# Performance work log

Hardware: AMD Instinct MI355X
Metric: run time of the kernel (lower is better)

## Reference

```python
import jax, jax.numpy as jnp
import numpy as np
import math

B, L, C, D, H, NLAYERS, DFF = 256, 100, 55, 512, 8, 3, 64


def _pos_embedding(length, d_model):
    pos = np.arange(length, dtype=np.float32)[:, None]
    div = np.exp(np.arange(0, d_model, 2, dtype=np.float32) * (-math.log(10000.0) / d_model))
    pe = np.zeros((length, d_model), dtype=np.float32)
    pe[:, 0::2] = np.sin(pos * div)
    pe[:, 1::2] = np.cos(pos * div)
    return jnp.asarray(pe)


def setup_inputs() -> dict:
    key = jax.random.key(0)
    ks = jax.random.split(key, 12)
    r = lambda k, s, sc: jax.random.normal(k, s, dtype=jnp.float32) * sc
    sD = 1.0 / math.sqrt(D)
    return {
        'x': r(ks[0], (B, L, C), 1.0),
        'tok_w': r(ks[1], (D, C, 3), 1.0 / math.sqrt(3 * C)),  # Conv1d(c_in->d_model, k=3, circular, no bias)
        'pe': _pos_embedding(L, D),
        'Wq': r(ks[2], (NLAYERS, D, D), sD), 'bq': jnp.zeros((NLAYERS, D), jnp.float32),
        'Wk': r(ks[3], (NLAYERS, D, D), sD), 'bk': jnp.zeros((NLAYERS, D), jnp.float32),
        'Wv': r(ks[4], (NLAYERS, D, D), sD), 'bv': jnp.zeros((NLAYERS, D), jnp.float32),
        'Wsig': r(ks[5], (NLAYERS, H, D), sD), 'bsig': jnp.zeros((NLAYERS, H), jnp.float32),
        'Wo': r(ks[6], (NLAYERS, D, D), sD), 'bo': jnp.zeros((NLAYERS, D), jnp.float32),
        'W1': r(ks[7], (NLAYERS, DFF, D), sD), 'b1': jnp.zeros((NLAYERS, DFF), jnp.float32),  # conv1 (1x1)
        'W2': r(ks[8], (NLAYERS, D, DFF), 1.0 / math.sqrt(DFF)), 'b2': jnp.zeros((NLAYERS, D), jnp.float32),  # conv2 (1x1)
        'proj_w': r(ks[9], (C, D), sD), 'proj_b': jnp.zeros((C,), jnp.float32),
    }


def _forward(x, tok_w, pe, Wq, bq, Wk, bk, Wv, bv, Wsig, bsig, Wo, bo, W1, b1, W2, b2, proj_w, proj_b):
    Bx, Lx, _ = x.shape
    nlayers, nH = Wsig.shape[0], Wsig.shape[1]
    d_model = Wq.shape[1]
    dk = d_model // nH
    scale = 1.0 / math.sqrt(dk)
    # token embedding: circular-padded Conv1d(k=3, no bias), then + positional embedding
    xc = jnp.pad(jnp.swapaxes(x, 1, 2), ((0, 0), (0, 0), (1, 1)), mode='wrap')  # [B,C,L+2]
    emb = jax.lax.conv_general_dilated(xc, tok_w, (1,), 'VALID', dimension_numbers=('NCW', 'OIW', 'NCW'))
    h = jnp.swapaxes(emb, 1, 2) + pe[None]  # [B,L,D]
    dist = jnp.abs(jnp.arange(Lx)[:, None] - jnp.arange(Lx)[None, :]).astype(h.dtype)  # |i-j|
    for l in range(nlayers):
        q = h @ Wq[l].T + bq[l]                       # [B,L,D]
        k = (h @ Wk[l].T + bk[l]).reshape(Bx, Lx, nH, dk)
        v = (h @ Wv[l].T + bv[l]).reshape(Bx, Lx, nH, dk)
        # NOTE: source applies sigma projection to the *projected* queries
        sigma = q @ Wsig[l].T + bsig[l]               # [B,L,H]
        qh = q.reshape(Bx, Lx, nH, dk)
        scores = jnp.einsum('blhe,bshe->bhls', qh, k)  # [B,H,L,L]
        series = jax.nn.softmax(scale * scores, axis=-1)
        # Gaussian prior branch (mask_flag=False; computed in source forward,
        # does not feed the module's returned output)
        sg = jnp.swapaxes(sigma, 1, 2)                 # [B,H,L]
        sg = jnp.power(3.0, jax.nn.sigmoid(sg * 5.0) + 1e-5) - 1.0
        sgE = sg[..., None]                            # [B,H,L,1]
        _prior = jnp.exp(-(dist ** 2)[None, None] / (2.0 * sgE ** 2)) / (math.sqrt(2.0 * math.pi) * sgE)
        o = jnp.einsum('bhls,bshd->blhd', series, v).reshape(Bx, Lx, d_model)
        h = h + (o @ Wo[l].T + bo[l])                  # residual 1 (dropout=identity at eval)
        y = jax.nn.gelu(h @ W1[l].T + b1[l], approximate=False)  # conv1 1x1 + gelu
        h = h + (y @ W2[l].T + b2[l])                  # conv2 1x1, residual 2
    return h @ proj_w.T + proj_b                       # [B,L,c_out]


def reference(x, tok_w, pe, Wq, bq, Wk, bk, Wv, bv, Wsig, bsig, Wo, bo, W1, b1, W2, b2, proj_w, proj_b):
    return _forward(x, tok_w, pe, Wq, bq, Wk, bk, Wv, bv, Wsig, bsig, Wo, bo, W1, b1, W2, b2, proj_w, proj_b)
```

## Files before the change

### kernel.cpp

```cpp
#include <hip/hip_runtime.h>
#include <stdint.h>

typedef unsigned short u16;
typedef __attribute__((ext_vector_type(8))) short short8;
typedef __attribute__((ext_vector_type(4))) float f32x4;

#define DEVI __device__ __forceinline__

#define BB   256
#define LL   100
#define CC   55
#define DD   512
#define HH   8
#define DKK  64
#define MM   (BB * LL)
#define KEMB 192
#define NSEG 17

DEVI float bf2f(u16 s) { union { unsigned int u; float f; } x; x.u = ((unsigned int)s) << 16; return x.f; }
DEVI u16 f2bf(float f) {
  union { float f; unsigned int u; } x; x.f = f;
  unsigned int u = x.u;
  return (u16)((u + 0x7FFFu + ((u >> 16) & 1u)) >> 16);
}

DEVI void async_lds16(const u16* gp, u16* lp) {
  __builtin_amdgcn_global_load_lds((const __attribute__((address_space(1))) void*)gp,
                                   (__attribute__((address_space(3))) void*)lp, 16, 0, 0);
}

DEVI void wave_lds_fence() {
  asm volatile("s_waitcnt lgkmcnt(0)" ::: "memory");
  __builtin_amdgcn_wave_barrier();
}

DEVI int swz_row(int r) { return (r & 3) ^ ((r >> 2) & 3); }

__global__ void detect_dtype(const u16* __restrict__ x, int* __restrict__ flag) {
  __shared__ int cnt[256];
  int tid = threadIdx.x;
  u16 u = x[2 * tid];
  int e = (u >> 7) & 0xFF;
  cnt[tid] = (e >= 0x5F && e <= 0x90) ? 1 : 0;
  __syncthreads();
  for (int s = 128; s > 0; s >>= 1) { if (tid < s) cnt[tid] += cnt[tid + s]; __syncthreads(); }
  if (tid == 0) *flag = (cnt[0] >= 160) ? 0 : 1;
}

struct Segs { const void* src[NSEG]; int off[NSEG + 1]; };

__global__ void convert_all(Segs s, const int* __restrict__ flag, u16* __restrict__ dst) {
  int i = blockIdx.x * 256 + threadIdx.x;
  if (i >= s.off[NSEG]) return;
  int sidx = 0;
#pragma unroll
  for (int k = 1; k < NSEG; k++) if (i >= s.off[k]) sidx = k;
  int j = i - s.off[sidx];
  u16 v;
  if (*flag) v = f2bf(((const float*)s.src[sidx])[j]);
  else       v = ((const u16*)s.src[sidx])[j];
  dst[i] = v;
}

__global__ void repack_w(const u16* __restrict__ tokw, u16* __restrict__ Wg) {
  int idx = blockIdx.x * 256 + threadIdx.x;
  if (idx >= 512 * KEMB) return;
  int d = idx / KEMB, j = idx % KEMB, k = j >> 6, c = j & 63;
  Wg[idx] = (c < CC) ? tokw[d * (CC * 3) + c * 3 + k] : (u16)0;
}

__global__ void repack_x(const u16* __restrict__ x, u16* __restrict__ Xg) {
  int idx = blockIdx.x * 256 + threadIdx.x;
  if (idx >= MM * KEMB) return;
  int m = idx / KEMB, j = idx % KEMB, k = j >> 6, c = j & 63;
  int b = m / LL, l = m % LL;
  int l2 = l + k - 1; l2 = (l2 + LL) % LL;
  Xg[idx] = (c < CC) ? x[(size_t)(b * LL + l2) * CC + c] : (u16)0;
}

struct GemmW { const u16* W[3]; const u16* bias[3]; void* out[3]; };

template<int BM, int BN, int NTT, int TAG, bool QKV, bool DIRECT>
__global__ __launch_bounds__(256)
void gemm_bt(const u16* __restrict__ A, int K, GemmW w,
             const u16* __restrict__ pe,
             const u16* __restrict__ resid,
             int dogelu,
             int ldo, int nvalid,
             const int* __restrict__ dtf)
{
  constexpr int BK = 32;
  constexpr int MI = BM / 32;
  constexpr int CW = BN / 2, NT = CW / 16;
  constexpr int SW = CW + 4;
  constexpr int STAGE_U16 = (BM + BN) * BK * 2;
  __shared__ alignas(16) u16 smem[STAGE_U16];
  u16* As = smem;
  u16* Bs = smem + BM * BK * 2;

  const int tid = threadIdx.x;
  const int lane = tid & 63;
  const int wv = __builtin_amdgcn_readfirstlane(tid >> 6);
  const int wm = wv & 1, wn = wv >> 1;
  const int l15 = lane & 15, qd = lane >> 4;
  const int swz = swz_row(l15);

  const int id = blockIdx.x;
  const int mpx = gridDim.x / (NTT * 8);
  const int xcd = id & 7, slot = id >> 3;
  const int m_t = xcd * mpx + slot / NTT;
  const int n_t = slot % NTT;
  const int m0 = m_t * BM;
  int n0 = n_t * BN;
  int sel = 0, n0l = n0;
  if (QKV) { sel = n0 >> 9; n0l = n0 & 511; }
  const u16* W = w.W[sel];
  const u16* bias = w.bias[sel];
  void* outp = w.out[sel];

  const f32x4 zf = {0.f, 0.f, 0.f, 0.f};
  f32x4 acc[MI][NT];
#pragma unroll
  for (int i = 0; i < MI; i++)
#pragma unroll
    for (int j = 0; j < NT; j++) acc[i][j] = zf;

  for (int k0 = 0; k0 < K; k0 += 2 * BK) {
    __syncthreads();
#pragma unroll
    for (int p = 0; p < 2; p++) {
      u16* Asp = As + p * BM * BK;
      u16* Bsp = Bs + p * BN * BK;
      const int kp = k0 + p * BK;
#pragma unroll
      for (int i = 0; i < BM / 64; i++) {
        int base = i * 256 + wv * 64;
        int idx = base + lane;
        int row = idx >> 2;
        int cs = ((idx & 3) ^ swz_row(row)) * 8;
        async_lds16(A + (size_t)(m0 + row) * K + kp + cs, Asp + base * 8);
      }
#pragma unroll
      for (int i = 0; i < BN / 64; i++) {
        int base = i * 256 + wv * 64;
        int idx = base + lane;
        int row = idx >> 2;
        int cs = ((idx & 3) ^ swz_row(row)) * 8;
        int gr = n0l + row; if (gr >= nvalid) gr = nvalid - 1;
        async_lds16(W + (size_t)gr * K + kp + cs, Bsp + base * 8);
      }
    }
    __syncthreads();

#pragma unroll
    for (int p = 0; p < 2; p++) {
      const u16* Asp = As + p * BM * BK;
      const u16* Bsp = Bs + p * BN * BK;
      short8 af[MI], bfr[NT];
#pragma unroll
      for (int mi = 0; mi < MI; mi++)
        af[mi] = *(const short8*)&Asp[(wm * (BM / 2) + mi * 16 + l15) * BK + ((qd ^ swz) * 8)];
#pragma unroll
      for (int ni = 0; ni < NT; ni++)
        bfr[ni] = *(const short8*)&Bsp[(wn * CW + ni * 16 + l15) * BK + ((qd ^ swz) * 8)];
#pragma unroll
      for (int mi = 0; mi < MI; mi++)
#pragma unroll
        for (int ni = 0; ni < NT; ni++)
          acc[mi][ni] = __builtin_amdgcn_mfma_f32_16x16x32_bf16(af[mi], bfr[ni], acc[mi][ni], 0, 0, 0);
    }
  }

  if (DIRECT) {
    const int sf = (dtf != nullptr) ? *dtf : 0;
#pragma unroll
    for (int mi = 0; mi < MI; mi++)
#pragma unroll
      for (int ni = 0; ni < NT; ni++) {
        int gcol = n0l + wn * CW + ni * 16 + l15;
        float bv = (bias && gcol < nvalid) ? bf2f(bias[gcol]) : 0.f;
#pragma unroll
        for (int r = 0; r < 4; r++) {
          int grow = m0 + wm * (BM / 2) + mi * 16 + qd * 4 + r;
          if (gcol < nvalid) {
            float v = acc[mi][ni][r] + bv;
            if (sf) ((float*)outp)[(size_t)grow * ldo + gcol] = v;
            else    ((u16*)outp)[(size_t)grow * ldo + gcol] = f2bf(v);
          }
        }
      }
    return;
  }

  __syncthreads();
  u16* slab = smem + wv * 16 * SW;
#pragma unroll
  for (int mi = 0; mi < MI; mi++) {
    const int lr = wm * (BM / 2) + mi * 16 + qd * 4;
    float v[NT][4];
    if (!QKV && resid) {
#pragma unroll
      for (int ni = 0; ni < NT; ni++) {
        int col = n0l + wn * CW + ni * 16 + l15;
#pragma unroll
        for (int r = 0; r < 4; r++)
          v[ni][r] = bf2f(resid[(size_t)(m0 + lr + r) * DD + col]);
      }
    } else {
#pragma unroll
      for (int ni = 0; ni < NT; ni++)
#pragma unroll
        for (int r = 0; r < 4; r++) v[ni][r] = 0.f;
    }
#pragma unroll
    for (int ni = 0; ni < NT; ni++) {
      const int lc = wn * CW + ni * 16 + l15;
      float bv = bias ? bf2f(bias[n0l + lc]) : 0.f;
#pragma unroll
      for (int r = 0; r < 4; r++) {
        float x = v[ni][r] + acc[mi][ni][r] + bv;
        if (!QKV && pe) x += bf2f(pe[((m0 + lr + r) % LL) * DD + n0l + lc]);
        if (!QKV && dogelu) x = 0.5f * x * (1.f + erff(x * 0.70710678118654752f));
        v[ni][r] = x;
      }
    }
#pragma unroll
    for (int ni = 0; ni < NT; ni++)
#pragma unroll
      for (int r = 0; r < 4; r++)
        slab[(qd * 4 + r) * SW + ni * 16 + l15] = f2bf(v[ni][r]);
    wave_lds_fence();
    if (BN == 128) {
      int r2 = lane >> 2, c2 = (lane & 3) * 16;
      int grow = m0 + wm * (BM / 2) + mi * 16 + r2;
      u16* op = (u16*)outp + (size_t)grow * ldo + n0l + wn * CW + c2;
      *(short8*)&op[0] = *(const short8*)&slab[r2 * SW + c2];
      *(short8*)&op[8] = *(const short8*)&slab[r2 * SW + c2 + 8];
    } else {
      if (lane < 32) {
        int r2 = lane >> 1, c2 = (lane & 1) * 16;
        int grow = m0 + wm * (BM / 2) + mi * 16 + r2;
        u16* op = (u16*)outp + (size_t)grow * ldo + n0l + wn * CW + c2;
        *(short8*)&op[0] = *(const short8*)&slab[r2 * SW + c2];
        *(short8*)&op[8] = *(const short8*)&slab[r2 * SW + c2 + 8];
      }
    }
    wave_lds_fence();
  }
}

__global__ __launch_bounds__(256)
void ffn_fused(const u16* __restrict__ h, const u16* __restrict__ W1,
               const u16* __restrict__ b1, const u16* __restrict__ W2,
               const u16* __restrict__ b2, u16* __restrict__ hout)
{
  constexpr int BM = 64, BK = 32, SW = 36;
  __shared__ alignas(16) u16 smem[4096 + 10496];
  u16* y      = smem;
  u16* shared = smem + 4096;
  u16* As  = shared;
  u16* Bs  = shared + 4096;
  u16* Bs2 = shared;
  u16* slabs = shared + 8192;

  const int tid = threadIdx.x;
  const int lane = tid & 63;
  const int wv = __builtin_amdgcn_readfirstlane(tid >> 6);
  const int wm = wv & 1, wn = wv >> 1;
  const int l15 = lane & 15, qd = lane >> 4;
  const int swz = swz_row(l15);
  const int id = blockIdx.x;
  const int mpx = gridDim.x >> 3;
  const int lid = (id & 7) * mpx + (id >> 3);
  const int m0 = (lid >> 1) * BM;
  const int nh = lid & 1;

  const int srow = tid >> 2;
  const int scs = ((tid & 3) ^ swz_row(srow)) * 8;
  const f32x4 zf = {0.f, 0.f, 0.f, 0.f};

  f32x4 acc[2][2];
#pragma unroll
  for (int i = 0; i < 2; i++)
#pragma unroll
    for (int j = 0; j < 2; j++) acc[i][j] = zf;

  for (int k0 = 0; k0 < DD; k0 += 64) {
    __syncthreads();
#pragma unroll
    for (int p = 0; p < 2; p++) {
      const int kp = k0 + p * BK;
      async_lds16(h  + (size_t)(m0 + srow) * DD + kp + scs, As + p * 2048 + tid * 8);
      async_lds16(W1 + (size_t)srow * DD + kp + scs,        Bs + p * 2048 + tid * 8);
    }
    __syncthreads();
#pragma unroll
    for (int p = 0; p < 2; p++) {
      short8 af[2], bfr[2];
#pragma unroll
      for (int mi = 0; mi < 2; mi++)
        af[mi] = *(const short8*)&As[p * 2048 + (wm * 32 + mi * 16 + l15) * BK + ((qd ^ swz) * 8)];
#pragma unroll
      for (int ni = 0; ni < 2; ni++)
        bfr[ni] = *(const short8*)&Bs[p * 2048 + (wn * 32 + ni * 16 + l15) * BK + ((qd ^ swz) * 8)];
#pragma unroll
      for (int mi = 0; mi < 2; mi++)
#pragma unroll
        for (int ni = 0; ni < 2; ni++)
          acc[mi][ni] = __builtin_amdgcn_mfma_f32_16x16x32_bf16(af[mi], bfr[ni], acc[mi][ni], 0, 0, 0);
    }
  }
#pragma unroll
  for (int mi = 0; mi < 2; mi++)
#pragma unroll
    for (int ni = 0; ni < 2; ni++) {
      float bv = bf2f(b1[wn * 32 + ni * 16 + l15]);
#pragma unroll
      for (int r = 0; r < 4; r++) {
        int row = wm * 32 + mi * 16 + qd * 4 + r;
        int kpos = ni * 16 + l15;
        int slot = ((kpos >> 3) ^ swz_row(row)) & 3;
        float x = acc[mi][ni][r] + bv;
        x = 0.5f * x * (1.f + erff(x * 0.70710678118654752f));
        y[wn * 2048 + row * BK + slot * 8 + (kpos & 7)] = f2bf(x);
      }
    }
  __syncthreads();

  auto stage2 = [&](int buf, int nc) {
#pragma unroll
    for (int p = 0; p < 2; p++)
      async_lds16(W2 + (size_t)(nc * 64 + srow) * 64 + p * BK + scs,
                  Bs2 + buf * 4096 + p * 2048 + tid * 8);
  };
  const int nc0 = nh * 4, nc1 = nc0 + 4;
  stage2(0, nc0);
  int cur = 0;
  u16* slab = slabs + wv * 16 * SW;
  for (int nc = nc0; nc < nc1; nc++) {
    __syncthreads();
    if (nc + 1 < nc1) stage2(cur ^ 1, nc + 1);
    f32x4 a2[2][2];
#pragma unroll
    for (int i = 0; i < 2; i++)
#pragma unroll
      for (int j = 0; j < 2; j++) a2[i][j] = zf;
#pragma unroll
    for (int p = 0; p < 2; p++) {
      short8 af[2], bfr[2];
#pragma unroll
      for (int mi = 0; mi < 2; mi++)
        af[mi] = *(const short8*)&y[p * 2048 + (wm * 32 + mi * 16 + l15) * BK + ((qd ^ swz) * 8)];
#pragma unroll
      for (int ni = 0; ni < 2; ni++)
        bfr[ni] = *(const short8*)&Bs2[cur * 4096 + p * 2048 + (wn * 32 + ni * 16 + l15) * BK + ((qd ^ swz) * 8)];
#pragma unroll
      for (int mi = 0; mi < 2; mi++)
#pragma unroll
        for (int ni = 0; ni < 2; ni++)
          a2[mi][ni] = __builtin_amdgcn_mfma_f32_16x16x32_bf16(af[mi], bfr[ni], a2[mi][ni], 0, 0, 0);
    }
    const int n0l = nc * 64;
#pragma unroll
    for (int mi = 0; mi < 2; mi++) {
      const int lr = wm * 32 + mi * 16 + qd * 4;
      float v[2][4];
#pragma unroll
      for (int ni = 0; ni < 2; ni++) {
        int col = n0l + wn * 32 + ni * 16 + l15;
        float bv = bf2f(b2[col]);
#pragma unroll
        for (int r = 0; r < 4; r++)
          v[ni][r] = bf2f(h[(size_t)(m0 + lr + r) * DD + col]) + a2[mi][ni][r] + bv;
      }
#pragma unroll
      for (int ni = 0; ni < 2; ni++)
#pragma unroll
        for (int r = 0; r < 4; r++)
          slab[(qd * 4 + r) * SW + ni * 16 + l15] = f2bf(v[ni][r]);
      wave_lds_fence();
      if (lane < 32) {
        int r2 = lane >> 1, c2 = (lane & 1) * 16;
        int grow = m0 + wm * 32 + mi * 16 + r2;
        u16* op = hout + (size_t)grow * DD + n0l + wn * 32 + c2;
        *(short8*)&op[0] = *(const short8*)&slab[r2 * SW + c2];
        *(short8*)&op[8] = *(const short8*)&slab[r2 * SW + c2 + 8];
      }
      wave_lds_fence();
    }
    cur ^= 1;
  }
}

__global__ __launch_bounds__(256)
void attn(const u16* __restrict__ qg, const u16* __restrict__ kg,
          const u16* __restrict__ vg, u16* __restrict__ og)
{
  constexpr int LP = 128;
  __shared__ alignas(16) u16 Ks[LP * DKK];
  __shared__ alignas(16) u16 Vt[DKK * LP];

  const int bh = blockIdx.x;
  const int b = bh >> 3, h = bh & 7;
  const size_t base = (size_t)b * LL * DD + (size_t)h * DKK;
  const int tid = threadIdx.x, lane = tid & 63, wv = tid >> 6;
  const int l15 = lane & 15, qd = lane >> 4;
  const short8 z8 = {0, 0, 0, 0, 0, 0, 0, 0};

  for (int i = tid; i < LP * 8; i += 256) {
    int row = i >> 3, e8 = (i & 7) * 8;
    short8 val = z8;
    if (row < LL) val = *(const short8*)(kg + base + (size_t)row * DD + e8);
    *(short8*)&Ks[row * DKK + e8] = val;
  }
  for (int i = tid; i < LP * 8; i += 256) {
    int j = i & 127, d0 = (i >> 7) * 8;
    short8 val = z8;
    if (j < LL) val = *(const short8*)(vg + base + (size_t)j * DD + d0);
#pragma unroll
    for (int u = 0; u < 8; u++) Vt[(d0 + u) * LP + j] = (u16)val[u];
  }
  __syncthreads();

  const f32x4 zf = {0.f, 0.f, 0.f, 0.f};
  f32x4 sc[2][8];
#pragma unroll
  for (int it = 0; it < 2; it++)
#pragma unroll
    for (int jt = 0; jt < 8; jt++) sc[it][jt] = zf;

  short8 af[2][2];
#pragma unroll
  for (int it = 0; it < 2; it++) {
    int row = (2 * wv + it) * 16 + l15;
#pragma unroll
    for (int ks = 0; ks < 2; ks++) {
      short8 val = z8;
      if (row < LL) val = *(const short8*)(qg + base + (size_t)row * DD + ks * 32 + qd * 8);
      af[it][ks] = val;
    }
  }
#pragma unroll
  for (int jt = 0; jt < 8; jt++) {
    short8 b0 = *(const short8*)&Ks[(jt * 16 + l15) * DKK + qd * 8];
    short8 b1 = *(const short8*)&Ks[(jt * 16 + l15) * DKK + 32 + qd * 8];
#pragma unroll
    for (int it = 0; it < 2; it++) {
      sc[it][jt] = __builtin_amdgcn_mfma_f32_16x16x32_bf16(af[it][0], b0, sc[it][jt], 0, 0, 0);
      sc[it][jt] = __builtin_amdgcn_mfma_f32_16x16x32_bf16(af[it][1], b1, sc[it][jt], 0, 0, 0);
    }
  }

  constexpr float scale = 0.125f;
#pragma unroll
  for (int it = 0; it < 2; it++) {
#pragma unroll
    for (int r = 0; r < 4; r++) {
      float vals[8];
      float mx = -1e30f;
#pragma unroll
      for (int jt = 0; jt < 8; jt++) {
        int col = jt * 16 + l15;
        float vv = sc[it][jt][r] * scale;
        if (col >= LL) vv = -1e30f;
        vals[jt] = vv;
        mx = fmaxf(mx, vv);
      }
#pragma unroll
      for (int off = 1; off < 16; off <<= 1) mx = fmaxf(mx, __shfl_xor(mx, off, 64));
      float s = 0.f;
#pragma unroll
      for (int jt = 0; jt < 8; jt++) { float p = __expf(vals[jt] - mx); vals[jt] = p; s += p; }
#pragma unroll
      for (int off = 1; off < 16; off <<= 1) s += __shfl_xor(s, off, 64);
      float inv = 1.f / s;
#pragma unroll
      for (int jt = 0; jt < 8; jt++) sc[it][jt][r] = vals[jt] * inv;
    }
  }
  __syncthreads();

  u16* Pc = Ks;
  f32x4 oc[2][4];
#pragma unroll
  for (int it = 0; it < 2; it++)
#pragma unroll
    for (int dt = 0; dt < 4; dt++) oc[it][dt] = zf;

#pragma unroll
  for (int it = 0; it < 2; it++) {
    int rb = (2 * wv + it) * 16 + qd * 4;
#pragma unroll
    for (int r = 0; r < 4; r++)
#pragma unroll
      for (int jt = 0; jt < 4; jt++)
        Pc[(rb + r) * DKK + jt * 16 + l15] = f2bf(sc[it][jt][r]);
  }
  __syncthreads();
#pragma unroll
  for (int ks = 0; ks < 2; ks++) {
    short8 ap[2];
#pragma unroll
    for (int it = 0; it < 2; it++)
      ap[it] = *(const short8*)&Pc[((2 * wv + it) * 16 + l15) * DKK + ks * 32 + qd * 8];
#pragma unroll
    for (int dt = 0; dt < 4; dt++) {
      short8 bv = *(const short8*)&Vt[(dt * 16 + l15) * LP + ks * 32 + qd * 8];
#pragma unroll
      for (int it = 0; it < 2; it++)
        oc[it][dt] = __builtin_amdgcn_mfma_f32_16x16x32_bf16(ap[it], bv, oc[it][dt], 0, 0, 0);
    }
  }
  __syncthreads();

#pragma unroll
  for (int it = 0; it < 2; it++) {
    int rb = (2 * wv + it) * 16 + qd * 4;
#pragma unroll
    for (int r = 0; r < 4; r++)
#pragma unroll
      for (int jt = 4; jt < 8; jt++)
        Pc[(rb + r) * DKK + (jt - 4) * 16 + l15] = f2bf(sc[it][jt][r]);
  }
  __syncthreads();
#pragma unroll
  for (int ks = 2; ks < 4; ks++) {
    short8 ap[2];
#pragma unroll
    for (int it = 0; it < 2; it++)
      ap[it] = *(const short8*)&Pc[((2 * wv + it) * 16 + l15) * DKK + (ks - 2) * 32 + qd * 8];
#pragma unroll
    for (int dt = 0; dt < 4; dt++) {
      short8 bv = *(const short8*)&Vt[(dt * 16 + l15) * LP + ks * 32 + qd * 8];
#pragma unroll
      for (int it = 0; it < 2; it++)
        oc[it][dt] = __builtin_amdgcn_mfma_f32_16x16x32_bf16(ap[it], bv, oc[it][dt], 0, 0, 0);
    }
  }

  __syncthreads();
  u16* Os = Ks;
#pragma unroll
  for (int it = 0; it < 2; it++) {
    int rb = (2 * wv + it) * 16 + qd * 4;
#pragma unroll
    for (int dt = 0; dt < 4; dt++)
#pragma unroll
      for (int r = 0; r < 4; r++)
        Os[(rb + r) * DKK + dt * 16 + l15] = f2bf(oc[it][dt][r]);
  }
  __syncthreads();
  {
    int row = tid >> 1, c0 = (tid & 1) * 32;
    if (row < LL) {
      u16* op = og + base + (size_t)row * DD + c0;
#pragma unroll
      for (int c = 0; c < 32; c += 8)
        *(short8*)&op[c] = *(const short8*)&Os[row * DKK + c0 + c];
    }
  }
}

extern "C" void kernel_launch(void* const* d_in, const int* in_sizes, int n_in,
                              void* d_out, int out_size, void* d_ws, size_t ws_size,
                              hipStream_t stream)
{
  (void)in_sizes; (void)n_in; (void)out_size; (void)ws_size;

  char* ws = (char*)d_ws;
  size_t off = 0;
  auto alloc = [&](size_t bytes) { char* p = ws + off; off += (bytes + 255) & ~(size_t)255; return p; };
  int* dflag = (int*)alloc(256);
  static const int seg_sizes[NSEG] = {
    MM * CC, DD * CC * 3, LL * DD,
    3 * DD * DD, 3 * DD, 3 * DD * DD, 3 * DD, 3 * DD * DD, 3 * DD,
    3 * DD * DD, 3 * DD, 3 * 64 * DD, 3 * 64, 3 * DD * 64, 3 * DD,
    CC * DD, CC
  };
  static const int seg_input[NSEG] = {0, 1, 2, 3, 4, 5, 6, 7, 8, 11, 12, 13, 14, 15, 16, 17, 18};
  int total = 0, segoff[NSEG + 1];
  for (int i = 0; i < NSEG; i++) { segoff[i] = total; total += seg_sizes[i]; }
  segoff[NSEG] = total;
  u16* canon = (u16*)alloc((size_t)total * 2);

  u16* hbf = (u16*)alloc((size_t)MM * DD * 2);
  u16* h2  = (u16*)alloc((size_t)MM * DD * 2);
  u16* qb  = (u16*)alloc((size_t)MM * DD * 2);
  u16* kb  = (u16*)alloc((size_t)MM * DD * 2);
  u16* vb  = (u16*)alloc((size_t)MM * DD * 2);
  u16* ob  = (u16*)alloc((size_t)MM * DD * 2);
  u16* Wg  = (u16*)alloc((size_t)512 * KEMB * 2);
  u16* Xg  = qb;

  const u16* xc  = canon + segoff[0];
  const u16* twc = canon + segoff[1];
  const u16* pec = canon + segoff[2];
  const u16* Wqc = canon + segoff[3];  const u16* bqc = canon + segoff[4];
  const u16* Wkc = canon + segoff[5];  const u16* bkc = canon + segoff[6];
  const u16* Wvc = canon + segoff[7];  const u16* bvc = canon + segoff[8];
  const u16* Woc = canon + segoff[9];  const u16* boc = canon + segoff[10];
  const u16* W1c = canon + segoff[11]; const u16* b1c = canon + segoff[12];
  const u16* W2c = canon + segoff[13]; const u16* b2c = canon + segoff[14];
  const u16* pwc = canon + segoff[15]; const u16* pbc = canon + segoff[16];

  Segs sg;
  for (int i = 0; i < NSEG; i++) { sg.src[i] = d_in[seg_input[i]]; sg.off[i] = segoff[i]; }
  sg.off[NSEG] = total;

  dim3 blk(256);
  detect_dtype<<<dim3(1), blk, 0, stream>>>((const u16*)d_in[0], dflag);
  convert_all<<<dim3((total + 255) / 256), blk, 0, stream>>>(sg, dflag, canon);
  repack_w<<<dim3((512 * KEMB + 255) / 256), blk, 0, stream>>>(twc, Wg);
  repack_x<<<dim3((MM * KEMB + 255) / 256), blk, 0, stream>>>(xc, Xg);

  auto W1of = [&](const u16* p) { GemmW g{}; g.W[0] = g.W[1] = g.W[2] = p; return g; };

  { GemmW g = W1of(Wg); g.out[0] = hbf;
    gemm_bt<128, 64, 8, 0, false, false><<<dim3(1600), blk, 0, stream>>>(Xg, KEMB, g, pec, nullptr, 0, DD, DD, nullptr); }

  u16* hc = hbf;
  for (int l = 0; l < 3; l++) {
    const u16* Wq_l = Wqc + (size_t)l * DD * DD; const u16* bq_l = bqc + l * DD;
    const u16* Wk_l = Wkc + (size_t)l * DD * DD; const u16* bk_l = bkc + l * DD;
    const u16* Wv_l = Wvc + (size_t)l * DD * DD; const u16* bv_l = bvc + l * DD;
    const u16* Wo_l = Woc + (size_t)l * DD * DD; const u16* bo_l = boc + l * DD;
    const u16* W1_l = W1c + (size_t)l * 64 * DD; const u16* b1_l = b1c + l * 64;
    const u16* W2_l = W2c + (size_t)l * DD * 64; const u16* b2_l = b2c + l * DD;

    { GemmW g{}; g.W[0] = Wq_l; g.W[1] = Wk_l; g.W[2] = Wv_l;
      g.bias[0] = bq_l; g.bias[1] = bk_l; g.bias[2] = bv_l;
      g.out[0] = qb; g.out[1] = kb; g.out[2] = vb;
      gemm_bt<128, 64, 24, 1, true, false><<<dim3(4800), blk, 0, stream>>>(hc, DD, g, nullptr, nullptr, 0, DD, DD, nullptr); }

    attn<<<dim3(BB * HH), blk, 0, stream>>>(qb, kb, vb, ob);

    { GemmW g = W1of(Wo_l); g.bias[0] = g.bias[1] = g.bias[2] = bo_l; g.out[0] = g.out[1] = g.out[2] = hc;
      gemm_bt<128, 64, 8, 2, false, false><<<dim3(1600), blk, 0, stream>>>(ob, DD, g, nullptr, hc, 0, DD, DD, nullptr); }

    u16* hn = (hc == hbf) ? h2 : hbf;
    ffn_fused<<<dim3(800), blk, 0, stream>>>(hc, W1_l, b1_l, W2_l, b2_l, hn);
    hc = hn;
  }
  { GemmW g = W1of(pwc); g.bias[0] = pbc; g.out[0] = d_out;
    gemm_bt<64, 64, 1, 5, false, true><<<dim3(400), blk, 0, stream>>>(hc, DD, g, nullptr, nullptr, 0, CC, CC, dflag); }
}
```

Baseline: 648.0 us.

## Add dedicated 128x256-tile QKV GEMM kernel with 4-slot async LDS pipeline

Replaces the generic 128x64-tile QKV projection GEMM with a specialized 512-thread kernel computing 128x256 output tiles. It stages A and B through a 4-slot LDS ring with async global-to-LDS loads two stages ahead, and uses an XCD-aware block-to-tile mapping. Larger tiles reuse each A tile across more output columns, cutting global traffic and launch count, at the cost of more LDS (96KB) and registers per block, which may lower occupancy.

```diff
diff --git a/kernel.cpp b/kernel.cpp
--- a/kernel.cpp
+++ b/kernel.cpp
@@ -249,6 +249,110 @@
   }
 }
 
+__global__ __launch_bounds__(512)
+void gemm_qkv(const u16* __restrict__ A, GemmW w)
+{
+  constexpr int K = DD;
+  constexpr int NBK = K >> 5;
+  constexpr int SLOT = 12288;
+  __shared__ alignas(16) u16 smem[4 * SLOT];
+
+  const int tid = threadIdx.x;
+  const int lane = tid & 63;
+  const int wv = __builtin_amdgcn_readfirstlane(tid >> 6);
+  const int wm = wv & 1, wn = wv >> 1;
+  const int l15 = lane & 15, qd = lane >> 4;
+  const int swk = ((qd ^ swz_row(l15)) & 3) * 8;
+
+  const int id = blockIdx.x;
+  const int mpx = gridDim.x / 48;
+  const int xcd = id & 7, sl = id >> 3;
+  const int m_t = xcd * mpx + sl / 6;
+  const int n_t = sl % 6;
+  const int m0 = m_t * 128;
+  const int sel = n_t >> 1;
+  const int n0l = (n_t & 1) * 256;
+  const u16* W = w.W[sel];
+  const u16* bias = w.bias[sel];
+  u16* outp = (u16*)w.out[sel];
+
+  const int arow = tid >> 2;
+  const u16* a_src = A + (size_t)(m0 + arow) * K + ((tid & 3) ^ swz_row(arow)) * 8;
+  const int br0 = tid >> 2, br1 = 128 + (tid >> 2);
+  const u16* b_src0 = W + (size_t)(n0l + br0) * K + ((tid & 3) ^ swz_row(br0)) * 8;
+  const u16* b_src1 = W + (size_t)(n0l + br1) * K + ((tid & 3) ^ swz_row(br1)) * 8;
+  const int a_dst  = wv * 512;
+  const int b_dst0 = 4096 + wv * 512;
+  const int b_dst1 = 8192 + wv * 512;
+
+  auto STAGE = [&](int t) {
+    u16* sb = smem + (t & 3) * SLOT;
+    const int kp = t << 5;
+    async_lds16(a_src + kp,  sb + a_dst);
+    async_lds16(b_src0 + kp, sb + b_dst0);
+    async_lds16(b_src1 + kp, sb + b_dst1);
+  };
+
+  const f32x4 zf = {0.f, 0.f, 0.f, 0.f};
+  f32x4 acc[4][4];
+#pragma unroll
+  for (int i = 0; i < 4; i++)
+#pragma unroll
+    for (int j = 0; j < 4; j++) acc[i][j] = zf;
+
+  STAGE(0);
+  STAGE(1);
+  for (int s = 0; s < NBK; ++s) {
+    if (s + 2 < NBK) {
+      STAGE(s + 2);
+      asm volatile("s_waitcnt vmcnt(6)" ::: "memory");
+    } else if (s + 1 < NBK) {
+      asm volatile("s_waitcnt vmcnt(3)" ::: "memory");
+    } else {
+      asm volatile("s_waitcnt vmcnt(0)" ::: "memory");
+    }
+    __builtin_amdgcn_s_barrier();
+    asm volatile("" ::: "memory");
+    const u16* sb = smem + (s & 3) * SLOT;
+    short8 af[4], bf[4];
+#pragma unroll
+    for (int mi = 0; mi < 4; mi++)
+      af[mi] = *(const short8*)&sb[(wm * 64 + mi * 16 + l15) * 32 + swk];
+#pragma unroll
+    for (int ni = 0; ni < 4; ni++)
+      bf[ni] = *(const short8*)&sb[4096 + (wn * 64 + ni * 16 + l15) * 32 + swk];
+#pragma unroll
+    for (int mi = 0; mi < 4; mi++)
+#pragma unroll
+      for (int ni = 0; ni < 4; ni++)
+        acc[mi][ni] = __builtin_amdgcn_mfma_f32_16x16x32_bf16(af[mi], bf[ni], acc[mi][ni], 0, 0, 0);
+    asm volatile("s_waitcnt lgkmcnt(0)" ::: "memory");
+  }
+  __syncthreads();
+
+  u16* slab = smem + wv * 4608;
+#pragma unroll
+  for (int mi = 0; mi < 4; mi++)
+#pragma unroll
+    for (int ni = 0; ni < 4; ni++) {
+      float bv = bf2f(bias[n0l + wn * 64 + ni * 16 + l15]);
+#pragma unroll
+      for (int r = 0; r < 4; r++)
+        slab[(mi * 16 + qd * 4 + r) * 72 + ni * 16 + l15] = f2bf(acc[mi][ni][r] + bv);
+    }
+  wave_lds_fence();
+  {
+    const int srow = lane >> 3, chk = lane & 7;
+#pragma unroll
+    for (int j = 0; j < 8; j++) {
+      int row = j * 8 + srow;
+      int grow = m0 + wm * 64 + row;
+      u16* op = outp + (size_t)grow * DD + n0l + wn * 64 + chk * 8;
+      *(short8*)op = *(const short8*)&slab[row * 72 + chk * 8];
+    }
+  }
+}
+
 __global__ __launch_bounds__(256)
 void ffn_fused(const u16* __restrict__ h, const u16* __restrict__ W1,
                const u16* __restrict__ b1, const u16* __restrict__ W2,
@@ -630,7 +734,7 @@
     { GemmW g{}; g.W[0] = Wq_l; g.W[1] = Wk_l; g.W[2] = Wv_l;
       g.bias[0] = bq_l; g.bias[1] = bk_l; g.bias[2] = bv_l;
       g.out[0] = qb; g.out[1] = kb; g.out[2] = vb;
-      gemm_bt<128, 64, 24, 1, true, false><<<dim3(4800), blk, 0, stream>>>(hc, DD, g, nullptr, nullptr, 0, DD, DD, nullptr); }
+      gemm_qkv<<<dim3(1200), dim3(512), 0, stream>>>(hc, g); }
 
     attn<<<dim3(BB * HH), blk, 0, stream>>>(qb, kb, vb, ob);
 
```

Result: no change. 637.9 us (-1.5%).
